# Kernel optimization log

Hardware: AMD Instinct MI355X
Metric: run time of the kernel (lower is better)

Reference implementation:

```python
import jax, jax.numpy as jnp
import numpy as np

N_ANGLES = 8


def setup_inputs() -> dict:
    key = jax.random.key(0)
    ks = jax.random.split(key, 6)
    N, in_size, out_size, K = 20000, 64, 64, 8
    M = N_ANGLES * N            # block-Laplacian dim = 160000
    E = M * 16                  # avg degree 16 -> 2.56M nnz
    x = jax.random.normal(ks[0], (N, in_size), dtype=jnp.float32)
    ls_vals = jax.random.normal(ks[1], (E,), dtype=jnp.float32) * 0.1
    ls_rows = jax.random.randint(ks[2], (E,), 0, M, dtype=jnp.int32)
    ls_cols = jax.random.randint(ks[3], (E,), 0, M, dtype=jnp.int32)
    weight = jax.random.normal(ks[4], (K, N_ANGLES * in_size, out_size), dtype=jnp.float32) * 0.05
    bias = jnp.zeros((out_size,), dtype=jnp.float32)
    return {"x": x, "ls_vals": ls_vals, "weight": weight, "bias": bias,
            "ls_rows": ls_rows, "ls_cols": ls_cols}


def reference(x, ls_vals, weight, bias, ls_rows, ls_cols):
    N, in_size = x.shape
    K = weight.shape[0]
    M = N_ANGLES * N

    def spmm(T):
        # sparse [M,M] @ dense [M,in] via gather + segment_sum
        return jax.ops.segment_sum(ls_vals[:, None] * T[ls_cols], ls_rows,
                                   num_segments=M)

    def feat(T):
        # [n_angles*N, in] -> [N, n_angles*in] (angle-major per node)
        return T.reshape(N_ANGLES, N, in_size).transpose(1, 0, 2).reshape(N, -1)

    Tx0 = jnp.tile(x, (N_ANGLES, 1))                  # [M, in]
    out = feat(Tx0) @ weight[0]                       # [N, out]
    Tx1 = spmm(Tx0)
    out = out + feat(Tx1) @ weight[1]
    for k in range(2, K):
        Tx2 = 2.0 * spmm(Tx1) - Tx0
        out = out + feat(Tx2) @ weight[k]
        Tx0, Tx1 = Tx1, Tx2
    return out + bias
```

## Files before the change

### kernel.cpp

```cpp
#include <hip/hip_runtime.h>
#include <hip/hip_bf16.h>

#define N_NODES 20000
#define NANG 8
#define CH 64
#define M_ROWS (NANG * N_NODES)
#define E_EDGES (M_ROWS * 16)
#define K_CHEB 8
#define WK_STRIDE (NANG * CH * CH)
#define BROWS 256
#define NB (M_ROWS / BROWS)
#define NCHUNK 1280
#define CHUNK (E_EDGES / NCHUNK)
#define SCAN_K (NCHUNK / 256)
#define RPW 4
#define SPMM_BLOCKS (M_ROWS / (4 * RPW))
#define KCAT 3648
#define SK_TOTAL 114
#define BCAP 5120
#define GROWS 32
#define GEMM_BLOCKS (N_NODES / GROWS)

typedef short short8 __attribute__((ext_vector_type(8)));
typedef float f32x4 __attribute__((ext_vector_type(4)));

__device__ __forceinline__ float bf2f(ushort u) {
    return __uint_as_float((unsigned int)u << 16);
}


__global__ __launch_bounds__(256) void count_kernel(const int* __restrict__ rows,
                                                    int* __restrict__ chunk_cnt) {
    __shared__ int h[NB];
    int c = blockIdx.x, tid = threadIdx.x;
    for (int i = tid; i < NB; i += 256) h[i] = 0;
    __syncthreads();
    int base = c * CHUNK;
    for (int i = tid; i < CHUNK; i += 256) atomicAdd(&h[rows[base + i] >> 8], 1);
    __syncthreads();
    for (int i = tid; i < NB; i += 256) chunk_cnt[(size_t)c * NB + i] = h[i];
}

__global__ __launch_bounds__(256) void bscan2_kernel(int* __restrict__ chunk_cnt,
                                                     int* __restrict__ btotal) {
    __shared__ int s[256];
    int b = blockIdx.x, t = threadIdx.x;
    int loc[SCAN_K];
    int sum = 0;
#pragma unroll
    for (int k = 0; k < SCAN_K; ++k) {
        loc[k] = chunk_cnt[(size_t)(t * SCAN_K + k) * NB + b];
        sum += loc[k];
    }
    s[t] = sum;
    __syncthreads();
#pragma unroll
    for (int off = 1; off < 256; off <<= 1) {
        int u = (t >= off) ? s[t - off] : 0;
        __syncthreads();
        s[t] += u;
        __syncthreads();
    }
    int run = s[t] - sum;
#pragma unroll
    for (int k = 0; k < SCAN_K; ++k) {
        chunk_cnt[(size_t)(t * SCAN_K + k) * NB + b] = run;
        run += loc[k];
    }
    if (t == 255) btotal[b] = s[255];
}

__global__ void bscan_kernel(const int* __restrict__ btotal, int* __restrict__ bstart) {
    __shared__ int s[1024];
    int t = threadIdx.x;
    int v = (t < NB) ? btotal[t] : 0;
    s[t] = v;
    __syncthreads();
    for (int off = 1; off < 1024; off <<= 1) {
        int u = (t >= off) ? s[t - off] : 0;
        __syncthreads();
        s[t] += u;
        __syncthreads();
    }
    if (t < NB) bstart[t] = s[t] - v;
    if (t == 1023) bstart[NB] = s[1023];
}

__global__ __launch_bounds__(256) void scatter_kernel(
        const int* __restrict__ rows, const int* __restrict__ cols,
        const float* __restrict__ vals, const int* __restrict__ chunk_cnt,
        const int* __restrict__ bstart, int2* __restrict__ bedges) {
    __shared__ int loff[NB];
    int c = blockIdx.x, tid = threadIdx.x;
    for (int i = tid; i < NB; i += 256)
        loff[i] = chunk_cnt[(size_t)c * NB + i] + bstart[i];
    __syncthreads();
    int base = c * CHUNK;
    for (int i = tid; i < CHUNK; i += 256) {
        int e = base + i;
        int r = rows[e];
        int p = atomicAdd(&loff[r >> 8], 1);
        bedges[p] = make_int2(cols[e] | ((r & 255) << 18), __float_as_int(vals[e]));
    }
}

__global__ __launch_bounds__(256) void bucket_group_kernel(
        const int* __restrict__ bstart, const int2* __restrict__ bin,
        int2* __restrict__ bout, int* __restrict__ row_start) {
    __shared__ int cnt[BROWS];
    __shared__ int pref[BROWS];
    __shared__ int fill[BROWS];
    __shared__ int2 ob[BCAP];
    int b = blockIdx.x, tid = threadIdx.x;
    int s = bstart[b], e = bstart[b + 1];
    int n = e - s;
    cnt[tid] = 0;
    __syncthreads();
    int2 eds[20];
    int ni = 0;
    for (int i = tid; i < n; i += 256, ++ni) {
        int2 ed = bin[s + i];
        if (ni < 20) eds[ni] = ed;
        atomicAdd(&cnt[(ed.x >> 18) & 255], 1);
    }
    __syncthreads();
    int v = cnt[tid];
    pref[tid] = v;
    __syncthreads();
#pragma unroll
    for (int off = 1; off < 256; off <<= 1) {
        int u = (tid >= off) ? pref[tid - off] : 0;
        __syncthreads();
        pref[tid] += u;
        __syncthreads();
    }
    int my_excl = pref[tid] - v;
    __syncthreads();
    pref[tid] = my_excl;
    fill[tid] = my_excl;
    __syncthreads();

    if (n <= BCAP) {
        ni = 0;
        for (int i = tid; i < n; i += 256, ++ni) {
            int2 ed = (ni < 20) ? eds[ni] : bin[s + i];
            int p = atomicAdd(&fill[(ed.x >> 18) & 255], 1);
            ob[p] = make_int2(ed.x & 0x3ffff, ed.y);
        }
        __syncthreads();
        for (int i = tid; i < n; i += 256)
            bout[s + i] = ob[i];
    } else {
        ni = 0;
        for (int i = tid; i < n; i += 256, ++ni) {
            int2 ed = (ni < 20) ? eds[ni] : bin[s + i];
            int p = atomicAdd(&fill[(ed.x >> 18) & 255], 1);
            bout[s + p] = make_int2(ed.x & 0x3ffff, ed.y);
        }
    }
    row_start[b * BROWS + tid] = s + pref[tid];
    if (b == NB - 1 && tid == 0) row_start[M_ROWS] = e;
}


__global__ void xconv_kernel(const float* __restrict__ x, ushort* __restrict__ xb) {
    int i = blockIdx.x * 256 + threadIdx.x;
    __hip_bfloat16 v = __float2bfloat16(x[i]);
    xb[i] = *(ushort*)&v;
}

__global__ void wcat_kernel(const float* __restrict__ W, ushort* __restrict__ Wcat) {
    int idx = blockIdx.x * 256 + threadIdx.x;
    int n   = idx / KCAT;
    int kkc = idx - n * KCAT;
    float v;
    if (kkc < 64) {
        v = 0.f;
#pragma unroll
        for (int a = 0; a < NANG; ++a) v += W[(a * 64 + kkc) * 64 + n];
    } else {
        int k  = ((kkc - 64) >> 9) + 1;
        int kk = (kkc - 64) & 511;
        v = W[(size_t)k * WK_STRIDE + kk * 64 + n];
    }
    __hip_bfloat16 b = __float2bfloat16(v);
    Wcat[idx] = *(ushort*)&b;
}


template <int TIN_TILED, int TSUB_MODE>
__global__ __launch_bounds__(256) void spmm_kernel(
        const int* __restrict__ row_start, const int2* __restrict__ edges,
        const ushort* __restrict__ Tin, const ushort* __restrict__ Tsub,
        ushort* __restrict__ Tout, float alpha, float beta) {
    int wid = (blockIdx.x * 256 + threadIdx.x) >> 6;
    int lane = threadIdx.x & 63;
    int r0 = wid * RPW;
    int l16 = lane & 15;

    int sb[RPW + 1];
#pragma unroll
    for (int j = 0; j <= RPW; ++j)
        sb[j] = __builtin_amdgcn_readfirstlane(row_start[r0 + j]);

    int2 ed[RPW];
#pragma unroll
    for (int j = 0; j < RPW; ++j) {
        int idx = min(sb[j] + l16, sb[j + 1] - 1);
        idx = max(idx, 0);
        ed[j] = edges[idx];
    }

#pragma unroll
    for (int j = 0; j < RPW; ++j) {
        int s = sb[j], e = sb[j + 1];
        float acc0 = 0.f, acc1 = 0.f;
        int2 cur = ed[j];
        for (int base = s; base < e; base += 16) {
            int2 nxt = cur;
            if (base + 16 < e) {
                int idx = min(base + 16 + l16, e - 1);
                nxt = edges[idx];
            }
            ushort raw[16];
#pragma unroll
            for (int i = 0; i < 16; ++i) {
                unsigned c = (unsigned)__builtin_amdgcn_readlane(cur.x, i);
                if (TIN_TILED) c %= N_NODES;
                raw[i] = Tin[(size_t)c * CH + lane];
            }
#pragma unroll
            for (int i = 0; i < 16; ++i) {
                int wbits = __builtin_amdgcn_readlane(cur.y, i);
                if (base + i >= e) wbits = 0;
                float t = bf2f(raw[i]);
                if (i & 1) acc1 = fmaf(__int_as_float(wbits), t, acc1);
                else       acc0 = fmaf(__int_as_float(wbits), t, acc0);
            }
            cur = nxt;
        }
        int r = r0 + j;
        float v = alpha * (acc0 + acc1);
        size_t oi = (size_t)r * CH + lane;
        if (TSUB_MODE == 1) v += beta * bf2f(Tsub[oi]);
        if (TSUB_MODE == 2) v += beta * bf2f(Tsub[(size_t)((unsigned)r % N_NODES) * CH + lane]);
        __hip_bfloat16 o = __float2bfloat16(v);
        Tout[oi] = *(ushort*)&o;
    }
}


__global__ __launch_bounds__(256) void gemm_cat_kernel(
        const ushort* __restrict__ xb,
        const ushort* __restrict__ Tall,
        const ushort* __restrict__ Wcat,
        const float* __restrict__ bias,
        float* __restrict__ out) {
    __shared__ float red[4][16][64];
    int m0 = blockIdx.x * GROWS;
    int w = threadIdx.x >> 6;
    int l = threadIdx.x & 63;
    int lm = l & 15;
    int lq = l >> 4;
    const short* Xp = (const short*)xb;
    const short* Tp = (const short*)Tall;
    const short* Wp = (const short*)Wcat;

    f32x4 acc[2][4];
#pragma unroll
    for (int rg = 0; rg < 2; ++rg)
#pragma unroll
        for (int t = 0; t < 4; ++t) acc[rg][t] = (f32x4){0.f, 0.f, 0.f, 0.f};

    auto LDA = [&](int sk, int rg) -> short8 {
        int u = sk - 2;
        return *(const short8*)(Tp
            + ((size_t)(u >> 4) * M_ROWS + (size_t)((u & 15) >> 1) * N_NODES
               + (m0 + rg * 16 + lm)) * CH
            + (u & 1) * 32 + lq * 8);
    };
    auto LDB = [&](int sk, int t) -> short8 {
        return *(const short8*)(Wp + (size_t)(t * 16 + lm) * KCAT + sk * 32 + lq * 8);
    };

    if (w == 0) {
#pragma unroll
        for (int sk = 0; sk < 2; ++sk) {
            short8 a0 = *(const short8*)(Xp + (size_t)(m0 + lm) * CH + sk * 32 + lq * 8);
            short8 a1 = *(const short8*)(Xp + (size_t)(m0 + 16 + lm) * CH + sk * 32 + lq * 8);
#pragma unroll
            for (int t = 0; t < 4; ++t) {
                short8 bf = LDB(sk, t);
                acc[0][t] = __builtin_amdgcn_mfma_f32_16x16x32_bf16(a0, bf, acc[0][t], 0, 0, 0);
                acc[1][t] = __builtin_amdgcn_mfma_f32_16x16x32_bf16(a1, bf, acc[1][t], 0, 0, 0);
            }
        }
    }

    int tb = 2 + w * 28;
#pragma unroll 2
    for (int i = 0; i < 28; ++i) {
        int sk = tb + i;
        short8 a0 = LDA(sk, 0);
        short8 a1 = LDA(sk, 1);
#pragma unroll
        for (int t = 0; t < 4; ++t) {
            short8 bf = LDB(sk, t);
            acc[0][t] = __builtin_amdgcn_mfma_f32_16x16x32_bf16(a0, bf, acc[0][t], 0, 0, 0);
            acc[1][t] = __builtin_amdgcn_mfma_f32_16x16x32_bf16(a1, bf, acc[1][t], 0, 0, 0);
        }
    }

#pragma unroll
    for (int rg = 0; rg < 2; ++rg) {
        if (rg) __syncthreads();
#pragma unroll
        for (int t = 0; t < 4; ++t)
#pragma unroll
            for (int rI = 0; rI < 4; ++rI) red[w][t * 4 + rI][l] = acc[rg][t][rI];
        __syncthreads();
        int col = w * 16 + lm;
        float b = bias[col];
#pragma unroll
        for (int rI = 0; rI < 4; ++rI) {
            int i2 = w * 4 + rI;
            float sum = red[0][i2][l] + red[1][i2][l] + red[2][i2][l] + red[3][i2][l];
            out[(size_t)(m0 + rg * 16 + lq * 4 + rI) * CH + col] = sum + b;
        }
    }
}


extern "C" void kernel_launch(void* const* d_in, const int* in_sizes, int n_in,
                              void* d_out, int out_size, void* d_ws, size_t ws_size,
                              hipStream_t stream) {
    (void)in_sizes; (void)n_in; (void)out_size; (void)ws_size;
    const float* x       = (const float*)d_in[0];
    const float* ls_vals = (const float*)d_in[1];
    const float* weight  = (const float*)d_in[2];
    const float* bias    = (const float*)d_in[3];
    const int*   ls_rows = (const int*)d_in[4];
    const int*   ls_cols = (const int*)d_in[5];
    float* out = (float*)d_out;

    char* ws = (char*)d_ws;
    size_t off = 0;
    auto alloc = [&](size_t bytes) -> void* {
        void* p = ws + off;
        off += (bytes + 255) & ~(size_t)255;
        return p;
    };
    int*  chunk_cnt = (int*)alloc((size_t)NCHUNK * NB * sizeof(int));
    int*  btotal    = (int*)alloc(NB * sizeof(int));
    int*  bstart    = (int*)alloc((NB + 1) * sizeof(int));
    int*  row_start = (int*)alloc((M_ROWS + 1) * sizeof(int));
    int2* bedges2   = (int2*)alloc((size_t)E_EDGES * sizeof(int2));
    ushort* Wcat = (ushort*)alloc((size_t)64 * KCAT * sizeof(ushort));
    ushort* xb   = (ushort*)alloc((size_t)N_NODES * CH * sizeof(ushort));
    ushort* Tall = (ushort*)alloc((size_t)7 * M_ROWS * CH * sizeof(ushort));
    int2* bedges = (int2*)Tall;

    count_kernel<<<NCHUNK, 256, 0, stream>>>(ls_rows, chunk_cnt);
    bscan2_kernel<<<NB, 256, 0, stream>>>(chunk_cnt, btotal);
    bscan_kernel<<<1, 1024, 0, stream>>>(btotal, bstart);
    scatter_kernel<<<NCHUNK, 256, 0, stream>>>(ls_rows, ls_cols, ls_vals, chunk_cnt,
                                               bstart, bedges);
    bucket_group_kernel<<<NB, 256, 0, stream>>>(bstart, bedges, bedges2, row_start);

    xconv_kernel<<<(N_NODES * CH) / 256, 256, 0, stream>>>(x, xb);
    wcat_kernel<<<(64 * KCAT) / 256, 256, 0, stream>>>(weight, Wcat);

    ushort* T[8];
    for (int k = 1; k < K_CHEB; ++k) T[k] = Tall + (size_t)(k - 1) * M_ROWS * CH;

    spmm_kernel<1, 0><<<SPMM_BLOCKS, 256, 0, stream>>>(
        row_start, bedges2, xb, xb, T[1], 1.f, 0.f);
    spmm_kernel<0, 2><<<SPMM_BLOCKS, 256, 0, stream>>>(
        row_start, bedges2, T[1], xb, T[2], 2.f, -1.f);
    for (int k = 3; k < K_CHEB; ++k) {
        spmm_kernel<0, 1><<<SPMM_BLOCKS, 256, 0, stream>>>(
            row_start, bedges2, T[k - 1], T[k - 2], T[k], 2.f, -1.f);
    }

    gemm_cat_kernel<<<GEMM_BLOCKS, 256, 0, stream>>>(xb, Tall, Wcat, bias, out);
}
```

Baseline: 615.6 us.

## Stage scatter edges in LDS by bucket for coalesced global writes

The scatter kernel now loads each chunk's edges into registers, builds a per-bucket histogram in shared memory, scans it, and places the edges into a bucket-sorted LDS staging buffer. It then writes them out contiguously per bucket, so global stores are coalesced instead of random per-edge writes. The chunk count drops so each block handles more edges, which gives longer contiguous runs. In exchange the kernel uses much more LDS per block, which lowers occupancy, and adds an extra block-level scan.

Result: faster. 572.6 us, median of 2 (-7.0%).

```diff
diff --git a/kernel.cpp b/kernel.cpp
--- a/kernel.cpp
+++ b/kernel.cpp
@@ -10,9 +10,10 @@
 #define WK_STRIDE (NANG * CH * CH)
 #define BROWS 256
 #define NB (M_ROWS / BROWS)
-#define NCHUNK 1280
+#define NCHUNK 512
 #define CHUNK (E_EDGES / NCHUNK)
 #define SCAN_K (NCHUNK / 256)
+#define SC_RE 20
 #define RPW 4
 #define SPMM_BLOCKS (M_ROWS / (4 * RPW))
 #define KCAT 3648
@@ -86,21 +87,80 @@
     if (t == 1023) bstart[NB] = s[1023];
 }
 
+
 __global__ __launch_bounds__(256) void scatter_kernel(
         const int* __restrict__ rows, const int* __restrict__ cols,
         const float* __restrict__ vals, const int* __restrict__ chunk_cnt,
         const int* __restrict__ bstart, int2* __restrict__ bedges) {
-    __shared__ int loff[NB];
+    __shared__ int2 stage[CHUNK];
+    __shared__ ushort bkey[CHUNK];
+    __shared__ int hist[NB];
+    __shared__ int fill[NB];
+    __shared__ int gaddr[NB];
+    __shared__ int sc[256];
     int c = blockIdx.x, tid = threadIdx.x;
-    for (int i = tid; i < NB; i += 256)
-        loff[i] = chunk_cnt[(size_t)c * NB + i] + bstart[i];
-    __syncthreads();
+    for (int i = tid; i < NB; i += 256) hist[i] = 0;
+    __syncthreads();
+
     int base = c * CHUNK;
+    int2 eds[SC_RE];
+    int keys[SC_RE];
+#pragma unroll
+    for (int k = 0; k < SC_RE; ++k) {
+        int i = tid + k * 256;
+        if (i < CHUNK) {
+            int e = base + i;
+            int r = rows[e];
+            eds[k] = make_int2(cols[e] | ((r & 255) << 18), __float_as_int(vals[e]));
+            keys[k] = r >> 8;
+            atomicAdd(&hist[keys[k]], 1);
+        } else keys[k] = -1;
+    }
+    __syncthreads();
+
+    int loc[3];
+    int sum = 0;
+    int b0 = tid * 3;
+#pragma unroll
+    for (int k = 0; k < 3; ++k) {
+        int b = b0 + k;
+        loc[k] = (b < NB) ? hist[b] : 0;
+        sum += loc[k];
+    }
+    sc[tid] = sum;
+    __syncthreads();
+#pragma unroll
+    for (int off = 1; off < 256; off <<= 1) {
+        int u = (tid >= off) ? sc[tid - off] : 0;
+        __syncthreads();
+        sc[tid] += u;
+        __syncthreads();
+    }
+    int run = sc[tid] - sum;
+#pragma unroll
+    for (int k = 0; k < 3; ++k) {
+        int b = b0 + k;
+        if (b < NB) {
+            fill[b] = run;
+            gaddr[b] = bstart[b] + chunk_cnt[(size_t)c * NB + b] - run;
+        }
+        run += loc[k];
+    }
+    __syncthreads();
+
+#pragma unroll
+    for (int k = 0; k < SC_RE; ++k) {
+        if (keys[k] >= 0) {
+            int p = atomicAdd(&fill[keys[k]], 1);
+            stage[p] = eds[k];
+            bkey[p] = (ushort)keys[k];
+        }
+    }
+    __syncthreads();
+
     for (int i = tid; i < CHUNK; i += 256) {
-        int e = base + i;
-        int r = rows[e];
-        int p = atomicAdd(&loff[r >> 8], 1);
-        bedges[p] = make_int2(cols[e] | ((r & 255) << 18), __float_as_int(vals[e]));
+        int b = bkey[i];
+        bedges[gaddr[b] + i] = stage[i];
     }
 }
 
```
